# Performance work log

Measured on AMD Instinct MI355X. Metric: run time of the kernel, lower is better.

Reference implementation:

```python
import jax, jax.numpy as jnp
import numpy as np

B = 4096       # batch_size
D = 128        # projection dim
TEMP = 0.5     # temperature
EPS = 1e-12    # F.normalize eps


def setup_inputs() -> dict:
    key = jax.random.key(0)
    k1, k2 = jax.random.split(key)
    zi = jax.random.normal(k1, (B, D), dtype=jnp.float32)
    zj = jax.random.normal(k2, (B, D), dtype=jnp.float32)
    return {"zi": zi, "zj": zj}


def _l2_normalize(x):
    n = jnp.sqrt(jnp.sum(x * x, axis=-1, keepdims=True))
    return x / jnp.maximum(n, EPS)


def reference(zi, zj):
    zi_n = _l2_normalize(zi)
    zj_n = _l2_normalize(zj)

    # four [B, B] similarity matrices
    lii = jnp.matmul(zi_n, zi_n.T) / TEMP
    lij = jnp.matmul(zi_n, zj_n.T) / TEMP
    lji = jnp.matmul(zj_n, zi_n.T) / TEMP
    ljj = jnp.matmul(zj_n, zj_n.T) / TEMP

    # positives: diagonal of ij and ji (row-major gather of ~mask == diagonal)
    pos = jnp.concatenate([jnp.diagonal(lij), jnp.diagonal(lji)], axis=0)[:, None]  # [2B, 1]

    # off-diagonal gather: for row r, columns != r (preserves row-major order of mask gather)
    r = jnp.arange(B)[:, None]          # [B, 1]
    c = jnp.arange(B - 1)[None, :]      # [1, B-1]
    cols = c + (c >= r).astype(c.dtype)  # [B, B-1]

    def offdiag(m):
        return jnp.take_along_axis(m, cols, axis=1)  # [B, B-1]

    neg_i = jnp.concatenate([offdiag(lii), offdiag(lij)], axis=1)  # [B, 2B-2]
    neg_j = jnp.concatenate([offdiag(lji), offdiag(ljj)], axis=1)  # [B, 2B-2]
    neg = jnp.concatenate([neg_i, neg_j], axis=0)                  # [2B, 2B-2]

    logits = jnp.concatenate([pos, neg], axis=1)                   # [2B, 2B-1]

    # cross-entropy with all labels == 0
    loss = jnp.mean(jax.nn.logsumexp(logits, axis=1) - logits[:, 0])
    return loss
```

## Files before the change

### kernel.cpp

```cpp
#include <hip/hip_runtime.h>
#include <hip/hip_bf16.h>

#define BATCH   4096
#define TWO_B   8192
#define DIM     128
#define INV_TEMP 2.0f
#define SFOLD 1.6986436f

typedef __attribute__((ext_vector_type(8))) short bf16x8;
typedef __attribute__((ext_vector_type(4))) float f32x4;

#define CS 16

#define ZB_BYTES   (TWO_B * DIM * 2)
#define RS_OFFSET  ZB_BYTES
#define PS_OFFSET  (RS_OFFSET + TWO_B * 4)

__global__ __launch_bounds__(256) void k_normalize(const float* __restrict__ zi,
                                                   const float* __restrict__ zj,
                                                   __hip_bfloat16* __restrict__ zb,
                                                   float* __restrict__ ps,
                                                   float* __restrict__ rowsum) {
    int w = threadIdx.x >> 6;
    int lane = threadIdx.x & 63;
    int r = blockIdx.x * 4 + w;

    if (threadIdx.x < 8) rowsum[blockIdx.x * 8 + threadIdx.x] = 0.0f;

    float2 vi = *reinterpret_cast<const float2*>(zi + (size_t)r * DIM + lane * 2);
    float2 vj = *reinterpret_cast<const float2*>(zj + (size_t)r * DIM + lane * 2);
    float ssi = vi.x * vi.x + vi.y * vi.y;
    float ssj = vj.x * vj.x + vj.y * vj.y;
    #pragma unroll
    for (int m = 1; m < 64; m <<= 1) {
        ssi += __shfl_xor(ssi, m, 64);
        ssj += __shfl_xor(ssj, m, 64);
    }
    float invi = 1.0f / fmaxf(sqrtf(ssi), 1e-12f);
    float invj = 1.0f / fmaxf(sqrtf(ssj), 1e-12f);

    float nix = vi.x * invi, niy = vi.y * invi;
    float njx = vj.x * invj, njy = vj.y * invj;

    __hip_bfloat162 hi2, hj2;
    hi2.x = __float2bfloat16(nix * SFOLD);
    hi2.y = __float2bfloat16(niy * SFOLD);
    hj2.x = __float2bfloat16(njx * SFOLD);
    hj2.y = __float2bfloat16(njy * SFOLD);
    *reinterpret_cast<__hip_bfloat162*>(zb + (size_t)r * DIM + lane * 2) = hi2;
    *reinterpret_cast<__hip_bfloat162*>(zb + (size_t)(r + BATCH) * DIM + lane * 2) = hj2;

    float d = nix * njx + niy * njy;
    #pragma unroll
    for (int m = 1; m < 64; m <<= 1) d += __shfl_xor(d, m, 64);

    __shared__ float red[4];
    if (lane == 0) red[w] = d;
    __syncthreads();
    if (threadIdx.x == 0)
        ps[blockIdx.x] = red[0] + red[1] + red[2] + red[3];
}

__global__ __launch_bounds__(256, 2) void k_sim(const __hip_bfloat16* __restrict__ zb,
                                                float* __restrict__ rowsum) {
    const int t = threadIdx.x;
    const int w = t >> 6;
    const int lane = t & 63;
    const int lo = lane & 15, hi = lane >> 4;

    const int rowBlock = blockIdx.x / CS;
    const int split    = blockIdx.x % CS;
    const int rowBase  = rowBlock * 256 + w * 64;

    const char* zbB = reinterpret_cast<const char*>(zb);

    bf16x8 a[4][4];
    #pragma unroll
    for (int i = 0; i < 4; ++i) {
        const char* rp = zbB + (size_t)(rowBase + i * 16 + lo) * 256 + hi * 16;
        #pragma unroll
        for (int ks = 0; ks < 4; ++ks)
            a[i][ks] = *reinterpret_cast<const bf16x8*>(rp + ks * 64);
    }

    float psum[4][4];
    #pragma unroll
    for (int i = 0; i < 4; ++i)
        #pragma unroll
        for (int p = 0; p < 4; ++p) psum[i][p] = 0.0f;

    for (int ct = 0; ct < 8; ++ct) {
        const int colBase = split * 512 + ct * 64;

        bf16x8 b[4][4];
        #pragma unroll
        for (int j = 0; j < 4; ++j) {
            const char* rp = zbB + (size_t)(colBase + j * 16 + lo) * 256 + hi * 16;
            #pragma unroll
            for (int ks = 0; ks < 4; ++ks)
                b[j][ks] = *reinterpret_cast<const bf16x8*>(rp + ks * 64);
        }

        f32x4 acc[4][4];
        #pragma unroll
        for (int i = 0; i < 4; ++i)
            #pragma unroll
            for (int j = 0; j < 4; ++j) acc[i][j] = (f32x4){0.f, 0.f, 0.f, 0.f};

        #pragma unroll
        for (int ks = 0; ks < 4; ++ks)
            #pragma unroll
            for (int i = 0; i < 4; ++i)
                #pragma unroll
                for (int j = 0; j < 4; ++j)
                    acc[i][j] = __builtin_amdgcn_mfma_f32_16x16x32_bf16(
                        a[i][ks], b[j][ks], acc[i][j], 0, 0, 0);

        if (colBase == rowBase) {
            #pragma unroll
            for (int i = 0; i < 4; ++i)
                #pragma unroll
                for (int p = 0; p < 4; ++p) {
                    float s = 0.0f;
                    #pragma unroll
                    for (int j = 0; j < 4; ++j) {
                        float e = exp2f(acc[i][j][p]);
                        if (j == i && lo == hi * 4 + p) e = 0.0f;
                        s += e;
                    }
                    psum[i][p] += s;
                }
        } else {
            #pragma unroll
            for (int i = 0; i < 4; ++i)
                #pragma unroll
                for (int p = 0; p < 4; ++p) {
                    float s = 0.0f;
                    #pragma unroll
                    for (int j = 0; j < 4; ++j) s += exp2f(acc[i][j][p]);
                    psum[i][p] += s;
                }
        }
    }

    #pragma unroll
    for (int i = 0; i < 4; ++i) {
        #pragma unroll
        for (int p = 0; p < 4; ++p) {
            float s = psum[i][p];
            s += __shfl_xor(s, 1, 64);
            s += __shfl_xor(s, 2, 64);
            s += __shfl_xor(s, 4, 64);
            s += __shfl_xor(s, 8, 64);
            if (lo == 0)
                atomicAdd(&rowsum[rowBase + i * 16 + hi * 4 + p], s);
        }
    }
}

__global__ __launch_bounds__(1024) void k_final(const float* __restrict__ rowsum,
                                                const float* __restrict__ ps,
                                                float* __restrict__ out) {
    __shared__ float redl[1024];
    __shared__ float redp[1024];
    const int t = threadIdx.x;

    float s = 0.0f;
    #pragma unroll
    for (int q = 0; q < TWO_B / 1024; ++q) s += logf(rowsum[t + q * 1024]);
    float p = ps[t];

    redl[t] = s;
    redp[t] = p;
    __syncthreads();
    #pragma unroll
    for (int off = 512; off > 0; off >>= 1) {
        if (t < off) {
            redl[t] += redl[t + off];
            redp[t] += redp[t + off];
        }
        __syncthreads();
    }
    if (t == 0)
        out[0] = (redl[0] - 2.0f * INV_TEMP * redp[0]) / (float)TWO_B;
}

extern "C" void kernel_launch(void* const* d_in, const int* in_sizes, int n_in,
                              void* d_out, int out_size, void* d_ws, size_t ws_size,
                              hipStream_t stream) {
    const float* zi = (const float*)d_in[0];
    const float* zj = (const float*)d_in[1];
    float* out = (float*)d_out;

    char* ws = (char*)d_ws;
    __hip_bfloat16* zb = (__hip_bfloat16*)ws;
    float* rowsum = (float*)(ws + RS_OFFSET);
    float* ps = (float*)(ws + PS_OFFSET);

    k_normalize<<<BATCH / 4, 256, 0, stream>>>(zi, zj, zb, ps, rowsum);
    k_sim<<<(TWO_B / 256) * CS, 256, 0, stream>>>(zb, rowsum);
    k_final<<<1, 1024, 0, stream>>>(rowsum, ps, out);
}
```

Baseline: 50.09 us.

## Exploit similarity matrix symmetry by computing only upper-triangular tile pairs

The full 2B x 2B similarity grid is replaced by the upper-triangular set of 256x256 tile pairs. Each off-diagonal tile feeds its exp sums both to its row sums and, through a shared-memory column accumulator and atomics, to the transposed rows. This roughly halves the MFMA and exp work. In exchange it adds column reductions, shared atomics and more global atomics, and each block now runs only two column tiles, so the row fragment load is amortised over less work.

```diff
diff --git a/kernel.cpp b/kernel.cpp
--- a/kernel.cpp
+++ b/kernel.cpp
@@ -10,7 +10,8 @@
 typedef __attribute__((ext_vector_type(8))) short bf16x8;
 typedef __attribute__((ext_vector_type(4))) float f32x4;
 
-#define CS 16
+#define NTB 32
+#define NPAIRS (NTB * (NTB + 1) / 2)
 
 #define ZB_BYTES   (TWO_B * DIM * 2)
 #define RS_OFFSET  ZB_BYTES
@@ -63,14 +64,25 @@
 
 __global__ __launch_bounds__(256, 2) void k_sim(const __hip_bfloat16* __restrict__ zb,
                                                 float* __restrict__ rowsum) {
+    __shared__ float colacc[128];
+
     const int t = threadIdx.x;
     const int w = t >> 6;
     const int lane = t & 63;
     const int lo = lane & 15, hi = lane >> 4;
 
-    const int rowBlock = blockIdx.x / CS;
-    const int split    = blockIdx.x % CS;
-    const int rowBase  = rowBlock * 256 + w * 64;
+    const int pair = blockIdx.x >> 1;
+    const int cs   = blockIdx.x & 1;
+    int rb = 0, accum = 0;
+    while (accum + (NTB - rb) <= pair) { accum += NTB - rb; ++rb; }
+    const int cb = rb + (pair - accum);
+    const bool offdiag = (rb != cb);
+
+    const int rowBase = rb * 256 + w * 64;
+    const int colWin  = cb * 256 + cs * 128;
+
+    if (t < 128) colacc[t] = 0.0f;
+    __syncthreads();
 
     const char* zbB = reinterpret_cast<const char*>(zb);
 
@@ -89,8 +101,9 @@
         #pragma unroll
         for (int p = 0; p < 4; ++p) psum[i][p] = 0.0f;
 
-    for (int ct = 0; ct < 8; ++ct) {
-        const int colBase = split * 512 + ct * 64;
+    #pragma unroll
+    for (int ct = 0; ct < 2; ++ct) {
+        const int colBase = colWin + ct * 64;
 
         bf16x8 b[4][4];
         #pragma unroll
@@ -116,30 +129,33 @@
                     acc[i][j] = __builtin_amdgcn_mfma_f32_16x16x32_bf16(
                         a[i][ks], b[j][ks], acc[i][j], 0, 0, 0);
 
-        if (colBase == rowBase) {
-            #pragma unroll
-            for (int i = 0; i < 4; ++i)
+        float cps[4] = {0.f, 0.f, 0.f, 0.f};
+        const bool diagTile = (colBase == rowBase);
+        #pragma unroll
+        for (int i = 0; i < 4; ++i) {
+            #pragma unroll
+            for (int p = 0; p < 4; ++p) {
+                float s = 0.0f;
                 #pragma unroll
-                for (int p = 0; p < 4; ++p) {
-                    float s = 0.0f;
-                    #pragma unroll
-                    for (int j = 0; j < 4; ++j) {
-                        float e = exp2f(acc[i][j][p]);
-                        if (j == i && lo == hi * 4 + p) e = 0.0f;
-                        s += e;
-                    }
-                    psum[i][p] += s;
+                for (int j = 0; j < 4; ++j) {
+                    float e = exp2f(acc[i][j][p]);
+                    if (diagTile && j == i && lo == hi * 4 + p) e = 0.0f;
+                    s += e;
+                    cps[j] += e;
                 }
-        } else {
-            #pragma unroll
-            for (int i = 0; i < 4; ++i)
-                #pragma unroll
-                for (int p = 0; p < 4; ++p) {
-                    float s = 0.0f;
-                    #pragma unroll
-                    for (int j = 0; j < 4; ++j) s += exp2f(acc[i][j][p]);
-                    psum[i][p] += s;
-                }
+                psum[i][p] += s;
+            }
+        }
+
+        if (offdiag) {
+            #pragma unroll
+            for (int j = 0; j < 4; ++j) {
+                float v = cps[j];
+                v += __shfl_xor(v, 16, 64);
+                v += __shfl_xor(v, 32, 64);
+                if (hi == 0)
+                    atomicAdd(&colacc[ct * 64 + j * 16 + lo], v);
+            }
         }
     }
 
@@ -156,6 +172,11 @@
                 atomicAdd(&rowsum[rowBase + i * 16 + hi * 4 + p], s);
         }
     }
+
+    if (offdiag) {
+        __syncthreads();
+        if (t < 128) atomicAdd(&rowsum[colWin + t], colacc[t]);
+    }
 }
 
 __global__ __launch_bounds__(1024) void k_final(const float* __restrict__ rowsum,
@@ -198,6 +219,6 @@
     float* ps = (float*)(ws + PS_OFFSET);
 
     k_normalize<<<BATCH / 4, 256, 0, stream>>>(zi, zj, zb, ps, rowsum);
-    k_sim<<<(TWO_B / 256) * CS, 256, 0, stream>>>(zb, rowsum);
+    k_sim<<<NPAIRS * 2, 256, 0, stream>>>(zb, rowsum);
     k_final<<<1, 1024, 0, stream>>>(rowsum, ps, out);
 }
```

Measured after the change: 55.36 us. +10.5%, slower.

## Double-buffer B tile loads in k_sim to overlap global loads with MFMA

Applied to the files above, without the earlier changes.

Splits each 64-column tile into two 32-column halves with separate register buffers, prefetching the next half while MFMAs and exp2 run on the current one. Fully unrolls the column loop and replaces the diagonal check with a per-element global row/column comparison. It is meant to hide global load latency behind compute, at the cost of more unrolled code and possible register pressure under the 2-waves launch bound.

```diff
diff --git a/kernel.cpp b/kernel.cpp
--- a/kernel.cpp
+++ b/kernel.cpp
@@ -68,9 +68,10 @@
     const int lane = t & 63;
     const int lo = lane & 15, hi = lane >> 4;
 
-    const int rowBlock = blockIdx.x / CS;
-    const int split    = blockIdx.x % CS;
+    const int rowBlock = blockIdx.x >> 4;
+    const int split    = blockIdx.x & (CS - 1);
     const int rowBase  = rowBlock * 256 + w * 64;
+    const int colWin   = split * 512;
 
     const char* zbB = reinterpret_cast<const char*>(zb);
 
@@ -89,59 +90,65 @@
         #pragma unroll
         for (int p = 0; p < 4; ++p) psum[i][p] = 0.0f;
 
-    for (int ct = 0; ct < 8; ++ct) {
-        const int colBase = split * 512 + ct * 64;
-
-        bf16x8 b[4][4];
-        #pragma unroll
-        for (int j = 0; j < 4; ++j) {
-            const char* rp = zbB + (size_t)(colBase + j * 16 + lo) * 256 + hi * 16;
-            #pragma unroll
-            for (int ks = 0; ks < 4; ++ks)
-                b[j][ks] = *reinterpret_cast<const bf16x8*>(rp + ks * 64);
-        }
-
-        f32x4 acc[4][4];
-        #pragma unroll
-        for (int i = 0; i < 4; ++i)
-            #pragma unroll
-            for (int j = 0; j < 4; ++j) acc[i][j] = (f32x4){0.f, 0.f, 0.f, 0.f};
-
-        #pragma unroll
-        for (int ks = 0; ks < 4; ++ks)
-            #pragma unroll
-            for (int i = 0; i < 4; ++i)
-                #pragma unroll
-                for (int j = 0; j < 4; ++j)
-                    acc[i][j] = __builtin_amdgcn_mfma_f32_16x16x32_bf16(
-                        a[i][ks], b[j][ks], acc[i][j], 0, 0, 0);
-
-        if (colBase == rowBase) {
-            #pragma unroll
-            for (int i = 0; i < 4; ++i)
-                #pragma unroll
-                for (int p = 0; p < 4; ++p) {
-                    float s = 0.0f;
-                    #pragma unroll
-                    for (int j = 0; j < 4; ++j) {
-                        float e = exp2f(acc[i][j][p]);
-                        if (j == i && lo == hi * 4 + p) e = 0.0f;
-                        s += e;
-                    }
-                    psum[i][p] += s;
-                }
-        } else {
-            #pragma unroll
-            for (int i = 0; i < 4; ++i)
-                #pragma unroll
-                for (int p = 0; p < 4; ++p) {
-                    float s = 0.0f;
-                    #pragma unroll
-                    for (int j = 0; j < 4; ++j) s += exp2f(acc[i][j][p]);
-                    psum[i][p] += s;
-                }
-        }
-    }
+    bf16x8 bA[2][4], bB[2][4];
+
+#define LOADB(bb, colBase)                                                     \
+    {                                                                          \
+        _Pragma("unroll")                                                      \
+        for (int j = 0; j < 2; ++j) {                                          \
+            const char* rp = zbB + (size_t)((colBase) + j * 16 + lo) * 256 +   \
+                             hi * 16;                                          \
+            _Pragma("unroll")                                                  \
+            for (int ks = 0; ks < 4; ++ks)                                     \
+                bb[j][ks] = *reinterpret_cast<const bf16x8*>(rp + ks * 64);    \
+        }                                                                      \
+    }
+
+#define COMPUTE(bb, colBase)                                                   \
+    {                                                                          \
+        f32x4 acc[4][2];                                                       \
+        _Pragma("unroll")                                                      \
+        for (int i = 0; i < 4; ++i) {                                          \
+            acc[i][0] = (f32x4){0.f, 0.f, 0.f, 0.f};                           \
+            acc[i][1] = (f32x4){0.f, 0.f, 0.f, 0.f};                           \
+        }                                                                      \
+        _Pragma("unroll")                                                      \
+        for (int ks = 0; ks < 4; ++ks)                                         \
+            for (int i = 0; i < 4; ++i) {                                      \
+                acc[i][0] = __builtin_amdgcn_mfma_f32_16x16x32_bf16(           \
+                    a[i][ks], bb[0][ks], acc[i][0], 0, 0, 0);                  \
+                acc[i][1] = __builtin_amdgcn_mfma_f32_16x16x32_bf16(           \
+                    a[i][ks], bb[1][ks], acc[i][1], 0, 0, 0);                  \
+            }                                                                  \
+        const bool mayDiag = ((unsigned)((colBase) - rowBase) < 64u);          \
+        _Pragma("unroll")                                                      \
+        for (int i = 0; i < 4; ++i) {                                          \
+            _Pragma("unroll")                                                  \
+            for (int p = 0; p < 4; ++p) {                                      \
+                int gr = rowBase + i * 16 + hi * 4 + p;                        \
+                float s = 0.0f;                                                \
+                _Pragma("unroll")                                              \
+                for (int j = 0; j < 2; ++j) {                                  \
+                    float e = exp2f(acc[i][j][p]);                             \
+                    if (mayDiag && gr == (colBase) + j * 16 + lo) e = 0.0f;    \
+                    s += e;                                                    \
+                }                                                              \
+                psum[i][p] += s;                                               \
+            }                                                                  \
+        }                                                                      \
+    }
+
+    LOADB(bA, colWin);
+    #pragma unroll
+    for (int cp = 0; cp < 8; ++cp) {
+        const int c0 = colWin + cp * 64;
+        LOADB(bB, c0 + 32);
+        COMPUTE(bA, c0);
+        if (cp < 7) LOADB(bA, c0 + 64);
+        COMPUTE(bB, c0 + 32);
+    }
+#undef LOADB
+#undef COMPUTE
 
     #pragma unroll
     for (int i = 0; i < 4; ++i) {
```

After: 137.0 us. 2.73x slower.
